# Performance work log

Hardware: AMD Instinct MI355X
Metric: run time of the kernel (lower is better)

Reference implementation:

```python
import jax, jax.numpy as jnp
import numpy as np

DIM = 768
NUM_HEADS = 16
HEAD_DIM = DIM // NUM_HEADS        # 48
AXIS_DIM = HEAD_DIM // 3           # 16 dims per spatial axis (t, y, x)
ROPE_BASE = 10000.0
T, H, W = 8, 14, 14                # N = 1568


def setup_inputs() -> dict:
    key = jax.random.key(0)
    k1, k2, k3 = jax.random.split(key, 3)
    B, N = 4, T * H * W
    x = jax.random.normal(k1, (B, N, DIM), dtype=jnp.float32)
    # 3D position grid (t, y, x) for each token
    t, y, xg = np.meshgrid(np.arange(T), np.arange(H), np.arange(W), indexing="ij")
    pos = jnp.asarray(np.stack([t.ravel(), y.ravel(), xg.ravel()], axis=-1), dtype=jnp.int32)  # [N,3]
    W_qkv = jax.random.normal(k2, (DIM, 3 * DIM), dtype=jnp.float32) * (DIM ** -0.5)
    W_proj = jax.random.normal(k3, (DIM, DIM), dtype=jnp.float32) * (DIM ** -0.5)
    b_proj = jnp.zeros((DIM,), dtype=jnp.float32)
    return {"x": x, "pos": pos, "W_qkv": W_qkv, "W_proj": W_proj, "b_proj": b_proj}


def _rope3d(q, k, pos):
    # q, k: [B, H, N, HEAD_DIM]; pos: [N, 3] int
    half = AXIS_DIM // 2  # 8 frequency pairs per axis
    inv_freq = ROPE_BASE ** (-jnp.arange(half, dtype=jnp.float32) / half)  # [half]
    # angles per axis: [N, 3, half]
    ang = pos.astype(jnp.float32)[:, :, None] * inv_freq[None, None, :]
    cos = jnp.cos(ang)  # [N, 3, half]
    sin = jnp.sin(ang)

    def rotate(t):
        # split head_dim into 3 axis chunks of AXIS_DIM, rotate_half within each
        t3 = t.reshape(*t.shape[:-1], 3, AXIS_DIM)          # [B,H,N,3,AXIS_DIM]
        t1, t2 = t3[..., :half], t3[..., half:]             # [B,H,N,3,half]
        c = cos[None, None]                                  # [1,1,N,3,half]
        s = sin[None, None]
        r = jnp.concatenate([t1 * c - t2 * s, t2 * c + t1 * s], axis=-1)
        return r.reshape(*t.shape)

    return rotate(q), rotate(k)


def reference(x, pos, W_qkv, W_proj, b_proj):
    B, N, C = x.shape
    scale = 1.0 / jnp.sqrt(jnp.asarray(HEAD_DIM, dtype=x.dtype))
    qkv = (x @ W_qkv).reshape(B, N, 3, NUM_HEADS, HEAD_DIM)
    qkv = jnp.transpose(qkv, (2, 0, 3, 1, 4))               # [3,B,H,N,Dh]
    q, k, v = qkv[0], qkv[1], qkv[2]
    q, k = _rope3d(q, k, pos)
    attn = jnp.einsum("bhnd,bhmd->bhnm", q, k) * scale      # [B,H,N,N]
    attn = jax.nn.softmax(attn, axis=-1)
    out = jnp.einsum("bhnm,bhmd->bhnd", attn, v)            # [B,H,N,Dh]
    out = jnp.transpose(out, (0, 2, 1, 3)).reshape(B, N, C)
    return out @ W_proj + b_proj
```

## Files before the change

### kernel.cpp

```cpp
#include <hip/hip_runtime.h>
#include <hip/hip_bf16.h>
#include <math.h>

#define DIM 768
#define NHEADS 16
#define HD 48
#define NTOK 1568
#define BATCH 4
#define ROWS (BATCH * NTOK)
#define QKV_COLS (3 * DIM)

typedef __attribute__((ext_vector_type(8))) _Float16 f16x8;
typedef __attribute__((ext_vector_type(2))) __fp16 fp16v2;
typedef __attribute__((ext_vector_type(4))) float f32x4;

__device__ inline ushort f2h(float f) {
    union { _Float16 h; ushort u; } v; v.h = (_Float16)f; return v.u;
}
__device__ inline float h2f(ushort u) {
    union { _Float16 h; ushort u; } v; v.u = u; return (float)v.h;
}

__device__ inline void gl16(const void* g, void* l) {
    __builtin_amdgcn_global_load_lds(
        (const __attribute__((address_space(1))) unsigned int*)g,
        (__attribute__((address_space(3))) unsigned int*)l, 16, 0, 0);
}

__global__ void cast_f32_f16(const float* __restrict__ in, ushort* __restrict__ out, int n4) {
    int i = blockIdx.x * blockDim.x + threadIdx.x;
    if (i >= n4) return;
    float4 v = ((const float4*)in)[i];
    ushort4 o;
    o.x = f2h(v.x); o.y = f2h(v.y); o.z = f2h(v.z); o.w = f2h(v.w);
    ((ushort4*)out)[i] = o;
}

__global__ void transpose_cast(const float* __restrict__ in, ushort* __restrict__ out,
                               int R, int C) {
    __shared__ ushort tile[32][33];
    int tx = threadIdx.x, ty = threadIdx.y;
    int c0 = blockIdx.x * 32, r0 = blockIdx.y * 32;
#pragma unroll
    for (int k = 0; k < 4; ++k)
        tile[ty + 8 * k][tx] = f2h(in[(size_t)(r0 + ty + 8 * k) * C + c0 + tx]);
    __syncthreads();
#pragma unroll
    for (int k = 0; k < 4; ++k)
        out[(size_t)(c0 + ty + 8 * k) * R + r0 + tx] = tile[tx][ty + 8 * k];
}

__global__ void transpose_v(const ushort* __restrict__ qkv, ushort* __restrict__ vt) {
    __shared__ ushort tile[32][33];
    int tx = threadIdx.x, ty = threadIdx.y;
    int c0 = blockIdx.x * 32, n0 = blockIdx.y * 32, b = blockIdx.z;
    const ushort* src = qkv + (size_t)b * NTOK * QKV_COLS + 2 * DIM;
#pragma unroll
    for (int k = 0; k < 4; ++k)
        tile[ty + 8 * k][tx] = src[(size_t)(n0 + ty + 8 * k) * QKV_COLS + c0 + tx];
    __syncthreads();
    ushort* dst = vt + (size_t)b * DIM * NTOK;
#pragma unroll
    for (int k = 0; k < 4; ++k)
        dst[(size_t)(c0 + ty + 8 * k) * NTOK + n0 + tx] = tile[tx][ty + 8 * k];
}

#define GBK 64

template <int BM>
__global__ __launch_bounds__(256) void gemm_f16(
    const ushort* __restrict__ A, const ushort* __restrict__ Bt,
    float* __restrict__ Cf, ushort* __restrict__ Cb,
    const float* __restrict__ bias, int M, int N, int K) {
    constexpr int MI = BM / 32;
    __shared__ ushort sA[2][BM * 64];
    __shared__ ushort sB[2][128 * 64];
    const int tid = threadIdx.x;
    const int wid = tid >> 6, lane = tid & 63;
    const int wm = wid >> 1, wn = wid & 1;
    const int m0 = blockIdx.y * BM, n0 = blockIdx.x * 128;
    const int lr = lane & 15, g = lane >> 4;

    auto STAGE = [&](int buf, int k0) {
#pragma unroll
        for (int i = 0; i < MI; ++i) {
            int c = tid + 256 * i;
            int row = c >> 3;
            int ch = (c & 7) ^ (row & 7);
            gl16(&A[(size_t)(m0 + row) * K + k0 + ch * 8], &sA[buf][(c & ~63) * 8]);
        }
#pragma unroll
        for (int i = 0; i < 4; ++i) {
            int c = tid + 256 * i;
            int row = c >> 3;
            int ch = (c & 7) ^ (row & 7);
            gl16(&Bt[(size_t)(n0 + row) * K + k0 + ch * 8], &sB[buf][(c & ~63) * 8]);
        }
    };

    f32x4 acc[MI][4] = {};
    const int NK = K / GBK;
    STAGE(0, 0);
    for (int t = 0; t < NK; ++t) {
        const int cur = t & 1;
        asm volatile("s_waitcnt vmcnt(0)" ::: "memory");
        __builtin_amdgcn_s_barrier();
        if (t + 1 < NK) STAGE(cur ^ 1, (t + 1) * GBK);
#pragma unroll
        for (int k2 = 0; k2 < GBK; k2 += 32) {
            f16x8 af[MI], bg[4];
#pragma unroll
            for (int f = 0; f < MI; ++f) {
                int ra = wm * (BM / 2) + f * 16 + lr;
                int ba = (ra * 128 + k2 * 2 + g * 16) ^ ((ra & 7) << 4);
                af[f] = *(const f16x8*)((const char*)sA[cur] + ba);
            }
#pragma unroll
            for (int f = 0; f < 4; ++f) {
                int rb = wn * 64 + f * 16 + lr;
                int bb = (rb * 128 + k2 * 2 + g * 16) ^ ((rb & 7) << 4);
                bg[f] = *(const f16x8*)((const char*)sB[cur] + bb);
            }
#pragma unroll
            for (int mi = 0; mi < MI; ++mi)
#pragma unroll
                for (int ni = 0; ni < 4; ++ni)
                    acc[mi][ni] = __builtin_amdgcn_mfma_f32_16x16x32_f16(
                        af[mi], bg[ni], acc[mi][ni], 0, 0, 0);
        }
    }
    const int cr = g * 4;
#pragma unroll
    for (int mi = 0; mi < MI; ++mi)
#pragma unroll
        for (int ni = 0; ni < 4; ++ni) {
            int col = n0 + wn * 64 + ni * 16 + lr;
#pragma unroll
            for (int j = 0; j < 4; ++j) {
                int row = m0 + wm * (BM / 2) + mi * 16 + cr + j;
                float v = acc[mi][ni][j];
                if (Cf) {
                    if (bias) v += bias[col];
                    Cf[(size_t)row * N + col] = v;
                } else {
                    Cb[(size_t)row * N + col] = f2h(v);
                }
            }
        }
}

__global__ void rope_f16(ushort* __restrict__ qkv, const int* __restrict__ pos) {
    int idx = blockIdx.x * blockDim.x + threadIdx.x;
    const int total = BATCH * NTOK * NHEADS * 3;
    if (idx >= total) return;
    int axis = idx % 3; int t = idx / 3;
    int h = t & 15; t >>= 4;
    int n = t % NTOK; int b = t / NTOK;

    float p = (float)pos[n * 3 + axis];
    size_t base = ((size_t)b * NTOK + n) * QKV_COLS + h * HD + axis * 16;

    ushort lo[8], hi[8], klo[8], khi[8];
    *(ushort4*)&lo[0] = *(ushort4*)&qkv[base];
    *(ushort4*)&lo[4] = *(ushort4*)&qkv[base + 4];
    *(ushort4*)&hi[0] = *(ushort4*)&qkv[base + 8];
    *(ushort4*)&hi[4] = *(ushort4*)&qkv[base + 12];
    *(ushort4*)&klo[0] = *(ushort4*)&qkv[base + DIM];
    *(ushort4*)&klo[4] = *(ushort4*)&qkv[base + DIM + 4];
    *(ushort4*)&khi[0] = *(ushort4*)&qkv[base + DIM + 8];
    *(ushort4*)&khi[4] = *(ushort4*)&qkv[base + DIM + 12];

    const float RINV = 0.31622776601683794f;
    float fj = 1.0f;
#pragma unroll
    for (int j = 0; j < 8; ++j) {
        float s, c; __sincosf(p * fj, &s, &c); fj *= RINV;
        float q1 = h2f(lo[j]), q2 = h2f(hi[j]);
        lo[j] = f2h(q1 * c - q2 * s);
        hi[j] = f2h(q2 * c + q1 * s);
        float k1 = h2f(klo[j]), k2 = h2f(khi[j]);
        klo[j] = f2h(k1 * c - k2 * s);
        khi[j] = f2h(k2 * c + k1 * s);
    }
    *(ushort4*)&qkv[base] = *(ushort4*)&lo[0];
    *(ushort4*)&qkv[base + 4] = *(ushort4*)&lo[4];
    *(ushort4*)&qkv[base + 8] = *(ushort4*)&hi[0];
    *(ushort4*)&qkv[base + 12] = *(ushort4*)&hi[4];
    *(ushort4*)&qkv[base + DIM] = *(ushort4*)&klo[0];
    *(ushort4*)&qkv[base + DIM + 4] = *(ushort4*)&klo[4];
    *(ushort4*)&qkv[base + DIM + 8] = *(ushort4*)&khi[0];
    *(ushort4*)&qkv[base + DIM + 12] = *(ushort4*)&khi[4];
}

#define QBLK 128
#define KVB 32
#define NT (NTOK / KVB)
#define PP 40

__global__ __launch_bounds__(256) void attn_mfma(const ushort* __restrict__ qkv,
                                                 const ushort* __restrict__ vt,
                                                 ushort* __restrict__ aout) {
    __shared__ ushort sK3[3][KVB * 64];
    __shared__ ushort sV3[3][64 * 32];
    __shared__ ushort sP[4][32 * PP];
    const int tid = threadIdx.x, w = tid >> 6, lane = tid & 63;
    const int b = blockIdx.x >> 4, h = blockIdx.x & 15;
    const int q0 = blockIdx.y * QBLK;
    const size_t bbase = (size_t)b * NTOK * QKV_COLS;
    const size_t vbase = ((size_t)b * DIM + h * HD) * NTOK;
    const int lr = lane & 15, g = lane >> 4, lk = g << 3;
    const float qs = 0.14433756729740643f * 1.4426950408889634f;
    const float M2 = 14.0f;

    if (tid < 32) {
        sV3[0][48 * 32 + tid] = 0x3C00;
        sV3[1][48 * 32 + tid] = 0x3C00;
        sV3[2][48 * 32 + tid] = 0x3C00;
    }
    asm volatile("s_waitcnt lgkmcnt(0)" ::: "memory");

    f16x8 aq[2][2];
#pragma unroll
    for (int rb = 0; rb < 2; ++rb) {
        int qr = q0 + w * 32 + rb * 16 + lr;
        if (qr >= NTOK) qr = NTOK - 1;
        const ushort* qp = &qkv[bbase + (size_t)qr * QKV_COLS + h * HD];
        ushort r0[8], r1[8];
        *(ushort4*)&r0[0] = *(const ushort4*)&qp[lk];
        *(ushort4*)&r0[4] = *(const ushort4*)&qp[lk + 4];
        if (g < 2) {
            *(ushort4*)&r1[0] = *(const ushort4*)&qp[32 + lk];
            *(ushort4*)&r1[4] = *(const ushort4*)&qp[32 + lk + 4];
        } else {
#pragma unroll
            for (int e = 0; e < 8; ++e) r1[e] = 0;
        }
        f16x8 a0, a1;
#pragma unroll
        for (int e = 0; e < 8; ++e) {
            a0[e] = (_Float16)(h2f(r0[e]) * qs);
            a1[e] = (_Float16)(h2f(r1[e]) * qs);
        }
        aq[rb][0] = a0; aq[rb][1] = a1;
    }

    auto STAGE = [&](int buf, int kv0) {
        {
            int c = tid, row = c >> 3;
            int ch = (c & 7) ^ (row & 7);
            gl16(&qkv[bbase + (size_t)(kv0 + row) * QKV_COLS + DIM + h * HD + ch * 8],
                 &sK3[buf][(c & ~63) * 8]);
        }
        if (lane < 48) {
            int c = w * 48 + lane, d = c >> 2;
            int cc = (c & 3) ^ ((d >> 1) & 3);
            gl16(&vt[vbase + (size_t)d * NTOK + kv0 + cc * 8],
                 &sV3[buf][w * 384]);
        }
    };

    f32x4 o[2][4] = {};

    STAGE(0, 0);
    STAGE(1, KVB);
    for (int t = 0; t < NT; ++t) {
        const int cur = t % 3;
        if (t + 1 < NT) asm volatile("s_waitcnt vmcnt(2)" ::: "memory");
        else            asm volatile("s_waitcnt vmcnt(0)" ::: "memory");
        __builtin_amdgcn_s_barrier();
        if (t + 2 < NT) STAGE((t + 2) % 3, (t + 2) * KVB);

        f16x8 bk[2][2];
#pragma unroll
        for (int f = 0; f < 2; ++f)
#pragma unroll
            for (int ks = 0; ks < 2; ++ks) {
                int row = f * 16 + lr;
                int byt = (row * 128 + ks * 64 + g * 16) ^ ((lr & 7) << 4);
                bk[f][ks] = *(const f16x8*)((const char*)sK3[cur] + byt);
            }
        f32x4 sacc[2][2] = {{{-M2, -M2, -M2, -M2}, {-M2, -M2, -M2, -M2}},
                            {{-M2, -M2, -M2, -M2}, {-M2, -M2, -M2, -M2}}};
        __builtin_amdgcn_s_setprio(1);
#pragma unroll
        for (int rb = 0; rb < 2; ++rb)
#pragma unroll
            for (int f = 0; f < 2; ++f) {
                sacc[rb][f] = __builtin_amdgcn_mfma_f32_16x16x32_f16(bk[f][0], aq[rb][0], sacc[rb][f], 0, 0, 0);
                sacc[rb][f] = __builtin_amdgcn_mfma_f32_16x16x32_f16(bk[f][1], aq[rb][1], sacc[rb][f], 0, 0, 0);
            }
        __builtin_amdgcn_s_setprio(0);

#pragma unroll
        for (int rb = 0; rb < 2; ++rb)
#pragma unroll
            for (int f = 0; f < 2; ++f) {
                float p[4];
#pragma unroll
                for (int j = 0; j < 4; ++j) {
                    float pv;
                    asm("v_exp_f32 %0, %1" : "=v"(pv) : "v"(sacc[rb][f][j]));
                    p[j] = pv;
                }
                union { fp16v2 h; uint u; } c0, c1;
                c0.h = __builtin_amdgcn_cvt_pkrtz(p[0], p[1]);
                c1.h = __builtin_amdgcn_cvt_pkrtz(p[2], p[3]);
                uint2 uu; uu.x = c0.u; uu.y = c1.u;
                *(uint2*)&sP[w][(rb * 16 + lr) * PP + f * 16 + 4 * g] = uu;
            }

        f16x8 bv[4];
#pragma unroll
        for (int nf = 0; nf < 4; ++nf) {
            int row = nf * 16 + lr;
            int byt = (row * 64 + g * 16) ^ (((lr >> 1) & 3) << 4);
            bv[nf] = *(const f16x8*)((const char*)sV3[cur] + byt);
        }
        __builtin_amdgcn_s_setprio(1);
#pragma unroll
        for (int rb = 0; rb < 2; ++rb) {
            f16x8 pa = *(const f16x8*)&sP[w][(rb * 16 + lr) * PP + lk];
#pragma unroll
            for (int nf = 0; nf < 4; ++nf)
                o[rb][nf] = __builtin_amdgcn_mfma_f32_16x16x32_f16(bv[nf], pa, o[rb][nf], 0, 0, 0);
        }
        __builtin_amdgcn_s_setprio(0);
    }

#pragma unroll
    for (int rb = 0; rb < 2; ++rb) {
        float lv = __shfl(o[rb][3][0], lr, 64);
        int qr = q0 + w * 32 + rb * 16 + lr;
        if (qr < NTOK) {
            float inv = 1.f / lv;
            size_t rbse = ((size_t)b * NTOK + qr) * DIM;
#pragma unroll
            for (int nf = 0; nf < 3; ++nf) {
                ushort4 h4;
#pragma unroll
                for (int j = 0; j < 4; ++j)
                    ((ushort*)&h4)[j] = f2h(o[rb][nf][j] * inv);
                *(ushort4*)&aout[rbse + h * HD + nf * 16 + 4 * g] = h4;
            }
        }
    }
}

extern "C" void kernel_launch(void* const* d_in, const int* in_sizes, int n_in,
                              void* d_out, int out_size, void* d_ws, size_t ws_size,
                              hipStream_t stream) {
    const float* x   = (const float*)d_in[0];
    const int*   pos = (const int*)d_in[1];
    const float* Wq  = (const float*)d_in[2];
    const float* Wp  = (const float*)d_in[3];
    const float* bp  = (const float*)d_in[4];
    float* out = (float*)d_out;

    ushort* ws     = (ushort*)d_ws;
    ushort* x_h    = ws;
    ushort* WqT    = x_h + (size_t)ROWS * DIM;
    ushort* WpT    = WqT + (size_t)QKV_COLS * DIM;
    ushort* qkv_h  = WpT + (size_t)DIM * DIM;
    ushort* aout   = qkv_h + (size_t)ROWS * QKV_COLS;
    ushort* vt     = x_h;

    cast_f32_f16<<<(ROWS * DIM / 4 + 255) / 256, 256, 0, stream>>>(x, x_h, ROWS * DIM / 4);
    transpose_cast<<<dim3(QKV_COLS / 32, DIM / 32), dim3(32, 8), 0, stream>>>(Wq, WqT, DIM, QKV_COLS);
    transpose_cast<<<dim3(DIM / 32, DIM / 32), dim3(32, 8), 0, stream>>>(Wp, WpT, DIM, DIM);

    gemm_f16<128><<<dim3(QKV_COLS / 128, ROWS / 128), 256, 0, stream>>>(
        x_h, WqT, nullptr, qkv_h, nullptr, ROWS, QKV_COLS, DIM);

    transpose_v<<<dim3(DIM / 32, NTOK / 32, BATCH), dim3(32, 8), 0, stream>>>(qkv_h, vt);

    rope_f16<<<(BATCH * NTOK * NHEADS * 3 + 255) / 256, 256, 0, stream>>>(qkv_h, pos);

    attn_mfma<<<dim3(BATCH * NHEADS, (NTOK + QBLK - 1) / QBLK), 256, 0, stream>>>(qkv_h, vt, aout);

    gemm_f16<64><<<dim3(DIM / 128, ROWS / 64), 256, 0, stream>>>(
        aout, WpT, out, nullptr, bp, ROWS, DIM, DIM);
}
```

Measured before the change: 152.7 us.

## Fuse V transpose into QKV GEMM epilogue and vectorize GEMM stores

Swaps the MFMA operand order so each lane holds four consecutive output columns, which allows packed half2 and float4 stores in the GEMM epilogue. Blocks that cover the V columns now write V directly in transposed layout into a separate buffer, so the standalone transpose_v kernel and one launch plus a full V read/write round trip go away. The transposed V writes are 2-byte scattered stores with an NTOK stride, which may be poorly coalesced. Vt moves to a fresh workspace region after aout instead of reusing x_h.

Result: faster. 145.1 us (-5.0%).

```diff
diff --git a/kernel.cpp b/kernel.cpp
--- a/kernel.cpp
+++ b/kernel.cpp
@@ -50,27 +50,12 @@
         out[(size_t)(c0 + ty + 8 * k) * R + r0 + tx] = tile[tx][ty + 8 * k];
 }
 
-__global__ void transpose_v(const ushort* __restrict__ qkv, ushort* __restrict__ vt) {
-    __shared__ ushort tile[32][33];
-    int tx = threadIdx.x, ty = threadIdx.y;
-    int c0 = blockIdx.x * 32, n0 = blockIdx.y * 32, b = blockIdx.z;
-    const ushort* src = qkv + (size_t)b * NTOK * QKV_COLS + 2 * DIM;
-#pragma unroll
-    for (int k = 0; k < 4; ++k)
-        tile[ty + 8 * k][tx] = src[(size_t)(n0 + ty + 8 * k) * QKV_COLS + c0 + tx];
-    __syncthreads();
-    ushort* dst = vt + (size_t)b * DIM * NTOK;
-#pragma unroll
-    for (int k = 0; k < 4; ++k)
-        dst[(size_t)(c0 + ty + 8 * k) * NTOK + n0 + tx] = tile[tx][ty + 8 * k];
-}
-
 #define GBK 64
 
 template <int BM>
 __global__ __launch_bounds__(256) void gemm_f16(
     const ushort* __restrict__ A, const ushort* __restrict__ Bt,
-    float* __restrict__ Cf, ushort* __restrict__ Cb,
+    float* __restrict__ Cf, ushort* __restrict__ Cb, ushort* __restrict__ Vt,
     const float* __restrict__ bias, int M, int N, int K) {
     constexpr int MI = BM / 32;
     __shared__ ushort sA[2][BM * 64];
@@ -126,27 +111,39 @@
 #pragma unroll
                 for (int ni = 0; ni < 4; ++ni)
                     acc[mi][ni] = __builtin_amdgcn_mfma_f32_16x16x32_f16(
-                        af[mi], bg[ni], acc[mi][ni], 0, 0, 0);
-        }
-    }
-    const int cr = g * 4;
-#pragma unroll
-    for (int mi = 0; mi < MI; ++mi)
+                        bg[ni], af[mi], acc[mi][ni], 0, 0, 0);
+        }
+    }
+    const bool vpath = (Vt != nullptr) && (n0 >= 2 * DIM);
+#pragma unroll
+    for (int mi = 0; mi < MI; ++mi) {
+        int m = m0 + wm * (BM / 2) + mi * 16 + lr;
 #pragma unroll
         for (int ni = 0; ni < 4; ++ni) {
-            int col = n0 + wn * 64 + ni * 16 + lr;
-#pragma unroll
-            for (int j = 0; j < 4; ++j) {
-                int row = m0 + wm * (BM / 2) + mi * 16 + cr + j;
-                float v = acc[mi][ni][j];
-                if (Cf) {
-                    if (bias) v += bias[col];
-                    Cf[(size_t)row * N + col] = v;
-                } else {
-                    Cb[(size_t)row * N + col] = f2h(v);
-                }
-            }
-        }
+            int nb = n0 + wn * 64 + ni * 16 + g * 4;
+            if (Cf) {
+                float4 b4 = *(const float4*)&bias[nb];
+                float4 o4;
+                o4.x = acc[mi][ni][0] + b4.x;
+                o4.y = acc[mi][ni][1] + b4.y;
+                o4.z = acc[mi][ni][2] + b4.z;
+                o4.w = acc[mi][ni][3] + b4.w;
+                *(float4*)&Cf[(size_t)m * N + nb] = o4;
+            } else if (vpath) {
+                int bb = m / NTOK, tok = m % NTOK;
+#pragma unroll
+                for (int j = 0; j < 4; ++j)
+                    Vt[((size_t)bb * DIM + (nb - 2 * DIM + j)) * NTOK + tok] =
+                        f2h(acc[mi][ni][j]);
+            } else {
+                union { fp16v2 h; uint u; } c0, c1;
+                c0.h = __builtin_amdgcn_cvt_pkrtz(acc[mi][ni][0], acc[mi][ni][1]);
+                c1.h = __builtin_amdgcn_cvt_pkrtz(acc[mi][ni][2], acc[mi][ni][3]);
+                uint2 uu; uu.x = c0.u; uu.y = c1.u;
+                *(uint2*)&Cb[(size_t)m * N + nb] = uu;
+            }
+        }
+    }
 }
 
 __global__ void rope_f16(ushort* __restrict__ qkv, const int* __restrict__ pos) {
@@ -362,21 +359,19 @@
     ushort* WpT    = WqT + (size_t)QKV_COLS * DIM;
     ushort* qkv_h  = WpT + (size_t)DIM * DIM;
     ushort* aout   = qkv_h + (size_t)ROWS * QKV_COLS;
-    ushort* vt     = x_h;
+    ushort* vt     = aout + (size_t)ROWS * DIM;
 
     cast_f32_f16<<<(ROWS * DIM / 4 + 255) / 256, 256, 0, stream>>>(x, x_h, ROWS * DIM / 4);
     transpose_cast<<<dim3(QKV_COLS / 32, DIM / 32), dim3(32, 8), 0, stream>>>(Wq, WqT, DIM, QKV_COLS);
     transpose_cast<<<dim3(DIM / 32, DIM / 32), dim3(32, 8), 0, stream>>>(Wp, WpT, DIM, DIM);
 
     gemm_f16<128><<<dim3(QKV_COLS / 128, ROWS / 128), 256, 0, stream>>>(
-        x_h, WqT, nullptr, qkv_h, nullptr, ROWS, QKV_COLS, DIM);
-
-    transpose_v<<<dim3(DIM / 32, NTOK / 32, BATCH), dim3(32, 8), 0, stream>>>(qkv_h, vt);
+        x_h, WqT, nullptr, qkv_h, vt, nullptr, ROWS, QKV_COLS, DIM);
 
     rope_f16<<<(BATCH * NTOK * NHEADS * 3 + 255) / 256, 256, 0, stream>>>(qkv_h, pos);
 
     attn_mfma<<<dim3(BATCH * NHEADS, (NTOK + QBLK - 1) / QBLK), 256, 0, stream>>>(qkv_h, vt, aout);
 
     gemm_f16<64><<<dim3(DIM / 128, ROWS / 64), 256, 0, stream>>>(
-        aout, WpT, out, nullptr, bp, ROWS, DIM, DIM);
-}
+        aout, WpT, out, nullptr, nullptr, bp, ROWS, DIM, DIM);
+}
```
